# Kernel tuning notes

Measured on AMD Instinct MI355X. Metric: run time of the kernel, lower is better.

Reference implementation:

```python
import jax, jax.numpy as jnp
import numpy as np


def _ring_mask(n, d, dtype):
    # concentric-square mask: ring index r = min(i, j, n-1-i, n-1-j);
    # outer d rings are 0, inner rings are 1; center forced to 1.
    i = jnp.arange(n)
    ri = jnp.minimum(i, n - 1 - i)  # [n]
    ring = jnp.minimum(ri[:, None], ri[None, :])  # [n, n]
    mask = (ring >= d).astype(dtype)
    w = (n + 1) // 2
    mask = mask.at[w - 1, w - 1].set(jnp.asarray(1, dtype))
    return mask


def _conv2d(x, w, b):
    # x: [B,1,2,C], w: [1,1,2,k] -> [B,1,1,C] (padding only along last axis)
    pad = (w.shape[3] - 1) // 2
    y = jax.lax.conv_general_dilated(
        x, w, window_strides=(1, 1), padding=((0, 0), (pad, pad)),
        dimension_numbers=('NCHW', 'OIHW', 'NCHW'))
    return y + b.reshape(1, 1, 1, 1)


def setup_inputs() -> dict:
    key = jax.random.key(0)
    k1, k2, k3, k4, k5 = jax.random.split(key, 5)
    B, C1, C2, P = 512, 16, 30, 15
    K = 5  # int((log2(480)+3)/2) made odd
    x = jax.random.normal(k1, (B, C1, C2, P, P), dtype=jnp.float32)
    w1 = jax.random.normal(k2, (1, 1, 2, K), dtype=jnp.float32) * 0.3
    b1 = jax.random.normal(k3, (1,), dtype=jnp.float32) * 0.1
    w2 = jax.random.normal(k4, (1, 1, 2, K), dtype=jnp.float32) * 0.3
    b2 = jax.random.normal(k5, (1,), dtype=jnp.float32) * 0.1
    return {"x": x, "w1": w1, "b1": b1, "w2": w2, "b2": b2}


def reference(x, w1, b1, w2, b2):
    B, C1, C2, H, W = x.shape
    C = C1 * C2
    out = x.reshape(B, C, H, W)
    d = (W - 1) // 2 - 1  # patch_size == W, ScaleMaskModule d
    mask = _ring_mask(W, d, x.dtype)  # [W, W]

    # masked branch: adaptive avg pool(1) == spatial mean of masked input
    out_x1 = (out * mask).mean(axis=(2, 3))  # [B, C]
    out_x2 = out_x1[:, ::-1]                 # reversed channel order
    out_xx = jnp.stack([out_x1, out_x2], axis=1)[:, None]  # [B,1,2,C]

    # plain branch
    out1 = out.mean(axis=(2, 3))  # [B, C]
    out2 = out1[:, ::-1]
    outx = jnp.stack([out1, out2], axis=1)[:, None]  # [B,1,2,C]

    a1 = jax.nn.sigmoid(_conv2d(outx, w1, b1))    # [B,1,1,C]
    a2 = jax.nn.sigmoid(_conv2d(out_xx, w2, b2))  # [B,1,1,C]
    at1 = jnp.transpose(a1 * a2, (0, 3, 1, 2))    # [B,C,1,1]
    at = jax.nn.sigmoid((at1 - 0.2) * 2)

    out = out * at
    return out.reshape(B, C1, C2, H, W)
```

## Files before the change

kernel.cpp:

```cpp
#include <hip/hip_runtime.h>
#include <math.h>

#define BB 512
#define CC 480
#define HW 225
#define CHW (CC * HW)
#define NF4 (CHW / 4)
#define NGRP (CC / 4)
#define NGRP_TOTAL (BB * NGRP)

#define RED_BLOCKS 1920
#define RED_THREADS 256
#define RED_WAVES (RED_BLOCKS * (RED_THREADS / 64))

#define CHUNKS 8
#define CHUNK_F4 (NF4 / CHUNKS)
#define CHUNK_CH (CC / CHUNKS)
#define SC_THREADS 256
#define SC_FULL_ITERS (CHUNK_F4 / SC_THREADS)
#define SC_TAIL (CHUNK_F4 - SC_FULL_ITERS * SC_THREADS)

using f4 = __attribute__((ext_vector_type(4))) float;

__device__ __forceinline__ float sigmoidf(float v) {
    return 1.0f / (1.0f + __expf(-v));
}

__global__ __launch_bounds__(RED_THREADS) void reduce_kernel(
    const float* __restrict__ x,
    float* __restrict__ S, float* __restrict__ R)
{
    const int wave = threadIdx.x >> 6;
    const int lane = threadIdx.x & 63;
    const int gw0 = blockIdx.x * (RED_THREADS / 64) + wave;

    for (int gg = gw0; gg < NGRP_TOTAL; gg += RED_WAVES) {
        const int b  = gg / NGRP;
        const int gr = gg - b * NGRP;
        const f4* __restrict__ gp = (const f4*)x + (long long)b * NF4 + gr * 225;

        float f0 = 0.f, f1 = 0.f, f2 = 0.f, f3 = 0.f;
        float r0 = 0.f, r1 = 0.f, r2 = 0.f, r3 = 0.f;
#pragma unroll
        for (int j = 0; j < 4; ++j) {
            const int idx = lane + 64 * j;
            if (idx < 225) {
                f4 v = gp[idx];
                const int e0 = 4 * idx;
#pragma unroll
                for (int jj = 0; jj < 4; ++jj) {
                    const int e = e0 + jj;
                    const float vv = v[jj];
                    const int q = (e >= 450) ? ((e >= 675) ? 3 : 2)
                                             : ((e >= 225) ? 1 : 0);
                    const int r = e - 225 * q;
                    const bool ring = (r >= 96 && r <= 98) ||
                                      (r >= 111 && r <= 113) ||
                                      (r >= 126 && r <= 128);
                    const float rv = ring ? vv : 0.f;
                    f0 += (q == 0) ? vv : 0.f;
                    f1 += (q == 1) ? vv : 0.f;
                    f2 += (q == 2) ? vv : 0.f;
                    f3 += (q == 3) ? vv : 0.f;
                    r0 += (q == 0) ? rv : 0.f;
                    r1 += (q == 1) ? rv : 0.f;
                    r2 += (q == 2) ? rv : 0.f;
                    r3 += (q == 3) ? rv : 0.f;
                }
            }
        }
#pragma unroll
        for (int off = 32; off > 0; off >>= 1) {
            f0 += __shfl_down(f0, off, 64);
            f1 += __shfl_down(f1, off, 64);
            f2 += __shfl_down(f2, off, 64);
            f3 += __shfl_down(f3, off, 64);
            r0 += __shfl_down(r0, off, 64);
            r1 += __shfl_down(r1, off, 64);
            r2 += __shfl_down(r2, off, 64);
            r3 += __shfl_down(r3, off, 64);
        }
        if (lane == 0) {
            const float s = 1.0f / 225.0f;
            const int base = b * CC + 4 * gr;
            S[base + 0] = f0 * s;  R[base + 0] = r0 * s;
            S[base + 1] = f1 * s;  R[base + 1] = r1 * s;
            S[base + 2] = f2 * s;  R[base + 2] = r2 * s;
            S[base + 3] = f3 * s;  R[base + 3] = r3 * s;
        }
    }
}

__global__ __launch_bounds__(512) void gate_kernel(
    const float* __restrict__ S, const float* __restrict__ R,
    const float* __restrict__ w1, const float* __restrict__ b1,
    const float* __restrict__ w2, const float* __restrict__ b2,
    float* __restrict__ G)
{
    const int b = blockIdx.x;
    const int c = threadIdx.x;
    if (c < CC) {
        const float* __restrict__ Ms = S + b * CC;
        const float* __restrict__ Rs = R + b * CC;
        float g1 = b1[0], g2 = b2[0];
#pragma unroll
        for (int k = 0; k < 5; ++k) {
            const int j = c + k - 2;
            if (j >= 0 && j < CC) {
                g1 += w1[k] * Ms[j] + w1[5 + k] * Ms[CC - 1 - j];
                g2 += w2[k] * Rs[j] + w2[5 + k] * Rs[CC - 1 - j];
            }
        }
        G[b * CC + c] = sigmoidf((sigmoidf(g1) * sigmoidf(g2) - 0.2f) * 2.0f);
    }
}

__global__ __launch_bounds__(SC_THREADS) void scale_kernel(
    const float* __restrict__ x, const float* __restrict__ G,
    float* __restrict__ out)
{
    __shared__ float As[CHUNK_CH];
    const int blk = blockIdx.x;
    const int b = blk >> 3;
    const int s = blk & 7;
    const int t = threadIdx.x;

    if (t < CHUNK_CH) As[t] = G[b * CC + s * CHUNK_CH + t];
    __syncthreads();

    const f4* __restrict__ xb = (const f4*)x + (long long)b * NF4 + s * CHUNK_F4;
    f4* __restrict__ ob = (f4*)out + (long long)b * NF4 + s * CHUNK_F4;

#pragma unroll 4
    for (int k = 0; k < SC_FULL_ITERS; ++k) {
        const int g = t + SC_THREADS * k;
        f4 v = xb[g];
        const int e = 4 * g;
        const int c = e / 225;
        const int rr = e - 225 * c;
        v[0] *= As[c];
        v[1] *= As[c + (rr >= 224)];
        v[2] *= As[c + (rr >= 223)];
        v[3] *= As[c + (rr >= 222)];
        __builtin_nontemporal_store(v, &ob[g]);
    }
    if (t < SC_TAIL) {
        const int g = SC_FULL_ITERS * SC_THREADS + t;
        f4 v = xb[g];
        const int e = 4 * g;
        const int c = e / 225;
        const int rr = e - 225 * c;
        v[0] *= As[c];
        v[1] *= As[c + (rr >= 224)];
        v[2] *= As[c + (rr >= 223)];
        v[3] *= As[c + (rr >= 222)];
        __builtin_nontemporal_store(v, &ob[g]);
    }
}

extern "C" void kernel_launch(void* const* d_in, const int* in_sizes, int n_in,
                              void* d_out, int out_size, void* d_ws, size_t ws_size,
                              hipStream_t stream)
{
    const float* x  = (const float*)d_in[0];
    const float* w1 = (const float*)d_in[1];
    const float* b1 = (const float*)d_in[2];
    const float* w2 = (const float*)d_in[3];
    const float* b2 = (const float*)d_in[4];
    float* out = (float*)d_out;

    float* S = (float*)d_ws;
    float* R = S + BB * CC;
    float* G = R + BB * CC;

    reduce_kernel<<<RED_BLOCKS, RED_THREADS, 0, stream>>>(x, S, R);
    gate_kernel<<<BB, 512, 0, stream>>>(S, R, w1, b1, w2, b2, G);
    scale_kernel<<<BB * CHUNKS, SC_THREADS, 0, stream>>>(x, G, out);
}
```

Before: 415.9 us.

## Simplify reduction to plain sums and compute ring sums in gate kernel

```diff
diff --git a/kernel.cpp b/kernel.cpp
--- a/kernel.cpp
+++ b/kernel.cpp
@@ -28,7 +28,7 @@
 
 __global__ __launch_bounds__(RED_THREADS) void reduce_kernel(
     const float* __restrict__ x,
-    float* __restrict__ S, float* __restrict__ R)
+    float* __restrict__ S)
 {
     const int wave = threadIdx.x >> 6;
     const int lane = threadIdx.x & 63;
@@ -40,33 +40,27 @@
         const f4* __restrict__ gp = (const f4*)x + (long long)b * NF4 + gr * 225;
 
         float f0 = 0.f, f1 = 0.f, f2 = 0.f, f3 = 0.f;
-        float r0 = 0.f, r1 = 0.f, r2 = 0.f, r3 = 0.f;
 #pragma unroll
         for (int j = 0; j < 4; ++j) {
             const int idx = lane + 64 * j;
             if (idx < 225) {
                 f4 v = gp[idx];
-                const int e0 = 4 * idx;
-#pragma unroll
-                for (int jj = 0; jj < 4; ++jj) {
-                    const int e = e0 + jj;
-                    const float vv = v[jj];
-                    const int q = (e >= 450) ? ((e >= 675) ? 3 : 2)
-                                             : ((e >= 225) ? 1 : 0);
-                    const int r = e - 225 * q;
-                    const bool ring = (r >= 96 && r <= 98) ||
-                                      (r >= 111 && r <= 113) ||
-                                      (r >= 126 && r <= 128);
-                    const float rv = ring ? vv : 0.f;
-                    f0 += (q == 0) ? vv : 0.f;
-                    f1 += (q == 1) ? vv : 0.f;
-                    f2 += (q == 2) ? vv : 0.f;
-                    f3 += (q == 3) ? vv : 0.f;
-                    r0 += (q == 0) ? rv : 0.f;
-                    r1 += (q == 1) ? rv : 0.f;
-                    r2 += (q == 2) ? rv : 0.f;
-                    r3 += (q == 3) ? rv : 0.f;
-                }
+                const float s1 = v[0] + v[1];
+                const float s2 = s1 + v[2];
+                const float hs = s2 + v[3];
+                const int q = (idx >= 113) ? ((idx >= 169) ? 3 : 2)
+                                           : ((idx >= 57) ? 1 : 0);
+                const float lo = (idx == 56) ? v[0]
+                               : (idx == 112) ? s1
+                               : (idx == 168) ? s2 : hs;
+                const float hi = hs - lo;
+                f0 += (q == 0) ? lo : 0.f;
+                f1 += (q == 1) ? lo : 0.f;
+                f2 += (q == 2) ? lo : 0.f;
+                f3 += (q == 3) ? lo : 0.f;
+                f1 += (q == 0) ? hi : 0.f;
+                f2 += (q == 1) ? hi : 0.f;
+                f3 += (q == 2) ? hi : 0.f;
             }
         }
 #pragma unroll
@@ -75,33 +69,40 @@
             f1 += __shfl_down(f1, off, 64);
             f2 += __shfl_down(f2, off, 64);
             f3 += __shfl_down(f3, off, 64);
-            r0 += __shfl_down(r0, off, 64);
-            r1 += __shfl_down(r1, off, 64);
-            r2 += __shfl_down(r2, off, 64);
-            r3 += __shfl_down(r3, off, 64);
         }
         if (lane == 0) {
             const float s = 1.0f / 225.0f;
             const int base = b * CC + 4 * gr;
-            S[base + 0] = f0 * s;  R[base + 0] = r0 * s;
-            S[base + 1] = f1 * s;  R[base + 1] = r1 * s;
-            S[base + 2] = f2 * s;  R[base + 2] = r2 * s;
-            S[base + 3] = f3 * s;  R[base + 3] = r3 * s;
+            S[base + 0] = f0 * s;
+            S[base + 1] = f1 * s;
+            S[base + 2] = f2 * s;
+            S[base + 3] = f3 * s;
         }
     }
 }
 
 __global__ __launch_bounds__(512) void gate_kernel(
-    const float* __restrict__ S, const float* __restrict__ R,
+    const float* __restrict__ x,
+    const float* __restrict__ S,
     const float* __restrict__ w1, const float* __restrict__ b1,
     const float* __restrict__ w2, const float* __restrict__ b2,
     float* __restrict__ G)
 {
+    __shared__ float Rs[CC];
     const int b = blockIdx.x;
     const int c = threadIdx.x;
+
+    if (c < CC) {
+        const float* __restrict__ ch = x + (long long)b * CHW + c * HW;
+        const float r = ((ch[96] + ch[97] + ch[98])
+                       + (ch[111] + ch[112] + ch[113]))
+                       + (ch[126] + ch[127] + ch[128]);
+        Rs[c] = r * (1.0f / 225.0f);
+    }
+    __syncthreads();
+
     if (c < CC) {
         const float* __restrict__ Ms = S + b * CC;
-        const float* __restrict__ Rs = R + b * CC;
         float g1 = b1[0], g2 = b2[0];
 #pragma unroll
         for (int k = 0; k < 5; ++k) {
@@ -170,10 +171,9 @@
     float* out = (float*)d_out;
 
     float* S = (float*)d_ws;
-    float* R = S + BB * CC;
-    float* G = R + BB * CC;
+    float* G = S + BB * CC;
 
-    reduce_kernel<<<RED_BLOCKS, RED_THREADS, 0, stream>>>(x, S, R);
-    gate_kernel<<<BB, 512, 0, stream>>>(S, R, w1, b1, w2, b2, G);
+    reduce_kernel<<<RED_BLOCKS, RED_THREADS, 0, stream>>>(x, S);
+    gate_kernel<<<BB, 512, 0, stream>>>(x, S, w1, b1, w2, b2, G);
     scale_kernel<<<BB * CHUNKS, SC_THREADS, 0, stream>>>(x, G, out);
 }
```

New measurement: 416.0 us. Within noise of the previous version (+0.0%).
